# Kernel optimization log

Measured on AMD Instinct MI355X. Metric: run time of the kernel, lower is better.

Reference implementation:

```python
import jax, jax.numpy as jnp
import numpy as np

N_NODES = 50000
N_EDGES = 800000
F_IN = 64
F_HID = 64
K = 3


def _cheb_norm(edge_index, edge_weight, n):
    # PyG ChebConv sym normalization with lambda_max=2: Lhat = -D^{-1/2} A D^{-1/2}
    # (diagonal of Lhat is exactly 0, so self-loop terms vanish)
    row, col = edge_index[0], edge_index[1]
    deg = jax.ops.segment_sum(edge_weight, row, num_segments=n)
    dis = jnp.where(deg > 0, jax.lax.rsqrt(jnp.where(deg > 0, deg, 1.0)), 0.0)
    return -dis[row] * edge_weight * dis[col]


def _prop(x, row, col, norm, n):
    # out[i] = sum_{e: col[e]=i} norm[e] * x[row[e]]
    return jax.ops.segment_sum(x[row] * norm[:, None], col, num_segments=n)


def _cheb_conv(x, W, b, row, col, norm, n):
    # ChebConv K=3: Tx0=x, Tx1=Lhat x, Tx2=2 Lhat Tx1 - Tx0
    tx0 = x
    tx1 = _prop(x, row, col, norm, n)
    tx2 = 2.0 * _prop(tx1, row, col, norm, n) - tx0
    return tx0 @ W[0] + tx1 @ W[1] + tx2 @ W[2] + b


def setup_inputs() -> dict:
    key = jax.random.key(0)
    ks = jax.random.split(key, 20)
    inp = {
        "x": jax.random.normal(ks[0], (N_NODES, F_IN), dtype=jnp.float32),
        "edge_index": jax.random.randint(ks[1], (2, N_EDGES), 0, N_NODES, dtype=jnp.int32),
        "edge_weight": jax.random.uniform(ks[2], (N_EDGES,), dtype=jnp.float32),
    }
    # 6 ChebConvs: x->gate (F_IN->F_HID) and h->gate (F_HID->F_HID) for z, r, h
    names_in = [("Wxz", "bxz", F_IN), ("Whz", "bhz", F_HID), ("Wxr", "bxr", F_IN),
                ("Whr", "bhr", F_HID), ("Wxh", "bxh", F_IN), ("Whh", "bhh", F_HID)]
    for i, (wn, bn, fin) in enumerate(names_in):
        scale = 1.0 / np.sqrt(fin)
        inp[wn] = jax.random.normal(ks[3 + i], (K, fin, F_HID), dtype=jnp.float32) * scale
        inp[bn] = jnp.zeros((F_HID,), dtype=jnp.float32)
    inp["Wlin"] = jax.random.normal(ks[12], (F_HID, 2), dtype=jnp.float32) * (1.0 / np.sqrt(F_HID))
    inp["blin"] = jnp.zeros((2,), dtype=jnp.float32)
    return inp


def reference(x, edge_index, edge_weight, Wxz, bxz, Whz, bhz, Wxr, bxr, Whr, bhr,
              Wxh, bxh, Whh, bhh, Wlin, blin):
    n = x.shape[0]
    row, col = edge_index[0], edge_index[1]
    norm = _cheb_norm(edge_index, edge_weight, n)
    h0 = jnp.zeros((n, F_HID), dtype=x.dtype)
    # GConvGRU single step (initial hidden state = 0)
    z = jax.nn.sigmoid(_cheb_conv(x, Wxz, bxz, row, col, norm, n)
                       + _cheb_conv(h0, Whz, bhz, row, col, norm, n))
    r = jax.nn.sigmoid(_cheb_conv(x, Wxr, bxr, row, col, norm, n)
                       + _cheb_conv(h0, Whr, bhr, row, col, norm, n))
    h_tilde = jnp.tanh(_cheb_conv(x, Wxh, bxh, row, col, norm, n)
                       + _cheb_conv(h0 * r, Whh, bhh, row, col, norm, n))
    h = z * h0 + (1.0 - z) * h_tilde
    # head: dropout in eval mode (identity) -> tanh -> linear -> sigmoid
    return jax.nn.sigmoid(jnp.tanh(h) @ Wlin + blin)
```

## Files before the change

kernel.cpp:

```cpp
#include <hip/hip_runtime.h>
#include <hip/hip_bf16.h>

#define N_NODES 50000
#define N_EDGES 800000
#define NB1 400
#define CH  2000
#define NBKT 196
#define CAP 8192
#define SORT_MAX 6144

typedef unsigned short ushort_t;
typedef unsigned long long u64;
typedef __attribute__((ext_vector_type(8))) short bf16x8;
typedef __attribute__((ext_vector_type(4))) float f32x4;

constexpr int GCUR_O  = 0;
constexpr int DIS_O   = 512;
constexpr int OFF_O   = 50512;
constexpr int CSLOT_O = 100544;
constexpr int RSLOT_O = 3311808;
constexpr int RW_O    = 4917440;
constexpr int ABUF_O  = 6517440;
constexpr int PBUF_O  = 11317440;
constexpr int XS_O    = CSLOT_O;
constexpr int T1S_O   = RSLOT_O;

__device__ __forceinline__ ushort_t f32_to_bf16(float f) {
    unsigned u = __float_as_uint(f);
    u += 0x7fffu + ((u >> 16) & 1u);
    return (ushort_t)(u >> 16);
}
__device__ __forceinline__ float bflo(unsigned u) { return __uint_as_float(u << 16); }
__device__ __forceinline__ float bfhi(unsigned u) { return __uint_as_float(u & 0xffff0000u); }
__device__ __forceinline__ unsigned packbf2(float a, float b) {
    return (unsigned)f32_to_bf16(a) | ((unsigned)f32_to_bf16(b) << 16);
}
__device__ __forceinline__ float fsigmoid(float x) { return 1.f / (1.f + __expf(-x)); }
__device__ __forceinline__ float ftanh(float x) {
    x = fminf(15.f, fmaxf(-15.f, x));
    float e = __expf(2.f * x);
    return (e - 1.f) / (e + 1.f);
}

__global__ __launch_bounds__(512) void k1(
    const int* __restrict__ ei, const float* __restrict__ ew,
    const float* __restrict__ x, const float* __restrict__ Wxz,
    const float* __restrict__ Wxh, unsigned* __restrict__ gcur,
    u64* __restrict__ cslot, unsigned* __restrict__ rslot,
    unsigned* __restrict__ abuf, ushort_t* __restrict__ pbuf) {
    int bid = blockIdx.x, t = threadIdx.x;
    if (bid < NB1) {
        __shared__ unsigned colbuf[CH], rowbuf[CH];
        __shared__ unsigned hc[256], hr[256], bc[256], br[256];
        if (t < 256) { hc[t] = 0; hr[t] = 0; }
        __syncthreads();
        int e0 = bid * CH;
        for (int i = t; i < CH; i += 512) {
            unsigned r = (unsigned)ei[e0 + i];
            unsigned c = (unsigned)ei[N_EDGES + e0 + i];
            rowbuf[i] = r;
            colbuf[i] = c;
            atomicAdd(&hc[c >> 8], 1u);
            atomicAdd(&hr[r >> 8], 1u);
        }
        __syncthreads();
        if (t < NBKT) {
            bc[t] = atomicAdd(&gcur[t], hc[t]);
            br[t] = atomicAdd(&gcur[256 + t], hr[t]);
        }
        __syncthreads();
        if (t < 256) { hc[t] = 0; hr[t] = 0; }
        __syncthreads();
        for (int i = t; i < CH; i += 512) {
            unsigned c = colbuf[i];
            unsigned r = rowbuf[i];
            unsigned w = __float_as_uint(ew[e0 + i]);
            unsigned dc = c >> 8;
            unsigned pc = bc[dc] + atomicAdd(&hc[dc], 1u);
            if (pc < CAP)
                cslot[dc * CAP + pc] = ((u64)w << 32) | ((c & 255u) << 16) | (r & 0xFFFFu);
            unsigned dr = r >> 8;
            unsigned pr = br[dr] + atomicAdd(&hr[dr], 1u);
            if (pr < CAP) rslot[dr * CAP + pr] = (w & 0xFFFFFF00u) | (r & 255u);
        }
    } else if (bid < NB1 + 98) {
        int n0 = (bid - NB1) * 512;
        for (int idx = t; idx < 512 * 32; idx += 512) {
            int n = n0 + (idx >> 5);
            if (n < N_NODES) {
                int q = idx & 31;
                float2 xv = ((const float2*)x)[n * 32 + q];
                abuf[n * 96 + q] = packbf2(xv.x, xv.y);
            }
        }
    } else {
        for (int idx = t; idx < 24576; idx += 512) {
            int k = idx >> 7, n = idx & 127;
            float v = (n < 64) ? Wxz[k * 64 + n] : Wxh[k * 64 + (n - 64)];
            int c = n >> 4, s = k >> 5, l = (((k >> 3) & 3) << 4) | (n & 15), j = k & 7;
            pbuf[((c * 6 + s) * 64 + l) * 8 + j] = f32_to_bf16(v);
        }
    }
}

__global__ __launch_bounds__(512) void k2(
    const float* __restrict__ x, const unsigned* __restrict__ gcur,
    const u64* __restrict__ cslot, const unsigned* __restrict__ rslot,
    float* __restrict__ dis, int* __restrict__ off,
    u64* __restrict__ rw, unsigned* __restrict__ xs) {
    int bid = blockIdx.x, t = threadIdx.x;
    __shared__ unsigned rawA[SORT_MAX], rawB[SORT_MAX];
    __shared__ unsigned hist[256], hsc[256], cur[256], gs[256];
    __shared__ float facc[256];

    if (t < 256) {
        gs[t] = (t < NBKT) ? gcur[t] : 0u;
        hist[t] = 0;
    }
    __syncthreads();
    for (int o = 1; o < 256; o <<= 1) {
        unsigned v = (t < 256 && t >= o) ? gs[t - o] : 0u;
        __syncthreads();
        if (t < 256) gs[t] += v;
        __syncthreads();
    }
    unsigned szb = gcur[bid];
    unsigned sz = min(szb, (unsigned)SORT_MAX);
    unsigned base = gs[bid] - szb;
    for (unsigned i = t; i < sz; i += 512) {
        u64 v = cslot[bid * CAP + i];
        unsigned lo = (unsigned)v;
        rawA[i] = lo;
        rawB[i] = (unsigned)(v >> 32);
        atomicAdd(&hist[(lo >> 16) & 255u], 1u);
    }
    __syncthreads();
    unsigned h0 = (t < 256) ? hist[t] : 0u;
    if (t < 256) hsc[t] = h0;
    __syncthreads();
    for (int o = 1; o < 256; o <<= 1) {
        unsigned v = (t < 256 && t >= o) ? hsc[t - o] : 0u;
        __syncthreads();
        if (t < 256) hsc[t] += v;
        __syncthreads();
    }
    if (t < 256) {
        hsc[t] -= h0;
        cur[t] = 0u;
        int c = bid * 256 + t;
        if (c <= N_NODES) off[c] = (int)(base + hsc[t]);
    }
    __syncthreads();
    for (unsigned i = t; i < sz; i += 512) {
        unsigned lo = rawA[i];
        unsigned d = (lo >> 16) & 255u;
        unsigned p = hsc[d] + atomicAdd(&cur[d], 1u);
        rw[base + p] = ((u64)rawB[i] << 32) | (lo & 0xFFFFu);
    }
    __syncthreads();

    if (t < 256) facc[t] = 0.f;
    __syncthreads();
    unsigned szr = min(gcur[256 + bid], (unsigned)CAP);
    for (unsigned i = t; i < szr; i += 512) {
        unsigned v = rslot[bid * CAP + i];
        atomicAdd(&facc[v & 255u], __uint_as_float(v & 0xFFFFFF00u));
    }
    __syncthreads();
    if (t < 256) {
        float d = facc[t];
        float r = d > 0.f ? rsqrtf(d) : 0.f;
        facc[t] = r;
        int n = bid * 256 + t;
        if (n < N_NODES) dis[n] = r;
    }
    __syncthreads();
    for (int idx = t; idx < 8192; idx += 512) {
        int nl = idx >> 5, q = idx & 31;
        int n = bid * 256 + nl;
        if (n < N_NODES) {
            float2 xv = ((const float2*)x)[n * 32 + q];
            float r = facc[nl];
            xs[n * 32 + q] = packbf2(r * xv.x, r * xv.y);
        }
    }
}

__global__ __launch_bounds__(256) void k_prop(
    const int* __restrict__ off, const u64* __restrict__ rw,
    const unsigned* __restrict__ xsrc, const float* __restrict__ dis,
    const float* __restrict__ xf, unsigned* __restrict__ abuf,
    unsigned* __restrict__ t1s, int mode) {
    int node = (blockIdx.x * 256 + threadIdx.x) >> 6;
    if (node >= N_NODES) return;
    int lane = threadIdx.x & 63, h = lane >> 5, q = lane & 31;
    int b = off[node], end = off[node + 1];
    float acc0 = 0.f, acc1 = 0.f;
    for (; b + 7 < end; b += 8) {
        u64 v0 = rw[b + h], v1 = rw[b + h + 2], v2 = rw[b + h + 4], v3 = rw[b + h + 6];
        unsigned r0 = (unsigned)v0 & 0xFFFFu, r1 = (unsigned)v1 & 0xFFFFu;
        unsigned r2 = (unsigned)v2 & 0xFFFFu, r3 = (unsigned)v3 & 0xFFFFu;
        float a0 = __uint_as_float((unsigned)(v0 >> 32));
        float a1 = __uint_as_float((unsigned)(v1 >> 32));
        float a2 = __uint_as_float((unsigned)(v2 >> 32));
        float a3 = __uint_as_float((unsigned)(v3 >> 32));
        unsigned u0 = xsrc[r0 * 32 + q], u1 = xsrc[r1 * 32 + q];
        unsigned u2 = xsrc[r2 * 32 + q], u3 = xsrc[r3 * 32 + q];
        acc0 += a0 * bflo(u0) + a1 * bflo(u1) + a2 * bflo(u2) + a3 * bflo(u3);
        acc1 += a0 * bfhi(u0) + a1 * bfhi(u1) + a2 * bfhi(u2) + a3 * bfhi(u3);
    }
    for (; b + 1 < end; b += 2) {
        u64 v = rw[b + h];
        unsigned r = (unsigned)v & 0xFFFFu;
        float a = __uint_as_float((unsigned)(v >> 32));
        unsigned u = xsrc[r * 32 + q];
        acc0 += a * bflo(u); acc1 += a * bfhi(u);
    }
    if (b < end && h == 0) {
        u64 v = rw[b];
        unsigned r = (unsigned)v & 0xFFFFu;
        float a = __uint_as_float((unsigned)(v >> 32));
        unsigned u = xsrc[r * 32 + q];
        acc0 += a * bflo(u); acc1 += a * bfhi(u);
    }
    acc0 += __shfl_xor(acc0, 32, 64);
    acc1 += __shfl_xor(acc1, 32, 64);
    if (h == 0) {
        float di = dis[node];
        float t0 = -di * acc0, t1v = -di * acc1;
        if (mode == 0) {
            abuf[node * 96 + 32 + q] = packbf2(t0, t1v);
            t1s[node * 32 + q] = packbf2(di * t0, di * t1v);
        } else {
            float2 xv = ((const float2*)xf)[node * 32 + q];
            abuf[node * 96 + 64 + q] = packbf2(2.f * t0 - xv.x, 2.f * t1v - xv.y);
        }
    }
}

__global__ __launch_bounds__(256) void k_gemm(
    const ushort_t* __restrict__ ab, const ushort_t* __restrict__ pbuf,
    const float* __restrict__ bxz, const float* __restrict__ bhz,
    const float* __restrict__ bxh, const float* __restrict__ bhh,
    const float* __restrict__ Wlin, const float* __restrict__ blin,
    float2* __restrict__ out) {
    __shared__ ushort_t bsh[24576];
    int tid = threadIdx.x;
    {
        uint4* s4 = (uint4*)bsh;
        const uint4* g4 = (const uint4*)pbuf;
        for (int i = tid; i < 3072; i += 256) s4[i] = g4[i];
    }
    __syncthreads();

    int wave = tid >> 6, lane = tid & 63;
    int quad = lane >> 4, m = lane & 15;
    int arow = blockIdx.x * 64 + wave * 16 + m;
    const ushort_t* ap = ab + (size_t)arow * 192 + quad * 8;

    f32x4 acc[8];
#pragma unroll
    for (int c = 0; c < 8; ++c) acc[c] = (f32x4){0.f, 0.f, 0.f, 0.f};
#pragma unroll
    for (int s = 0; s < 6; ++s) {
        bf16x8 af = *(const bf16x8*)(ap + s * 32);
#pragma unroll
        for (int c = 0; c < 8; ++c) {
            bf16x8 bfr = *(const bf16x8*)(bsh + ((c * 6 + s) * 64 + lane) * 8);
            acc[c] = __builtin_amdgcn_mfma_f32_16x16x32_bf16(af, bfr, acc[c], 0, 0, 0);
        }
    }
    float bzv[4], bhv[4], wl0[4], wl1[4];
#pragma unroll
    for (int c = 0; c < 4; ++c) {
        int col = c * 16 + m;
        bzv[c] = bxz[col] + bhz[col];
        bhv[c] = bxh[col] + bhh[col];
        wl0[c] = Wlin[2 * col];
        wl1[c] = Wlin[2 * col + 1];
    }
    float bl0 = blin[0], bl1 = blin[1];
#pragma unroll
    for (int i = 0; i < 4; ++i) {
        float p0 = 0.f, p1 = 0.f;
#pragma unroll
        for (int c = 0; c < 4; ++c) {
            float z  = fsigmoid(acc[c][i] + bzv[c]);
            float ht = ftanh(acc[c + 4][i] + bhv[c]);
            float t  = ftanh((1.f - z) * ht);
            p0 += t * wl0[c];
            p1 += t * wl1[c];
        }
        for (int o = 1; o <= 8; o <<= 1) {
            p0 += __shfl_xor(p0, o, 64);
            p1 += __shfl_xor(p1, o, 64);
        }
        int g = blockIdx.x * 64 + wave * 16 + quad * 4 + i;
        if (m == 0 && g < N_NODES)
            out[g] = make_float2(fsigmoid(p0 + bl0), fsigmoid(p1 + bl1));
    }
}

extern "C" void kernel_launch(void* const* d_in, const int* in_sizes, int n_in,
                              void* d_out, int out_size, void* d_ws, size_t ws_size,
                              hipStream_t stream) {
    const float* x    = (const float*)d_in[0];
    const int*   ei   = (const int*)d_in[1];
    const float* ew   = (const float*)d_in[2];
    const float* Wxz  = (const float*)d_in[3];
    const float* bxz  = (const float*)d_in[4];
    const float* bhz  = (const float*)d_in[6];
    const float* Wxh  = (const float*)d_in[11];
    const float* bxh  = (const float*)d_in[12];
    const float* bhh  = (const float*)d_in[14];
    const float* Wlin = (const float*)d_in[15];
    const float* blin = (const float*)d_in[16];

    float*    ws    = (float*)d_ws;
    unsigned* gcur  = (unsigned*)(ws + GCUR_O);
    float*    dis   = ws + DIS_O;
    int*      off   = (int*)(ws + OFF_O);
    u64*      cslot = (u64*)(ws + CSLOT_O);
    unsigned* rslot = (unsigned*)(ws + RSLOT_O);
    u64*      rw    = (u64*)(ws + RW_O);
    unsigned* abuf  = (unsigned*)(ws + ABUF_O);
    ushort_t* pbuf  = (ushort_t*)(ws + PBUF_O);
    unsigned* xs    = (unsigned*)(ws + XS_O);
    unsigned* t1s   = (unsigned*)(ws + T1S_O);

    hipMemsetAsync(d_ws, 0, 512 * 4, stream);

    k1<<<NB1 + 98 + 1, 512, 0, stream>>>(ei, ew, x, Wxz, Wxh, gcur, cslot, rslot, abuf, pbuf);
    k2<<<NBKT, 512, 0, stream>>>(x, gcur, cslot, rslot, dis, off, rw, xs);
    k_prop<<<12500, 256, 0, stream>>>(off, rw, xs, dis, x, abuf, t1s, 0);
    k_prop<<<12500, 256, 0, stream>>>(off, rw, t1s, dis, x, abuf, abuf, 1);
    k_gemm<<<782, 256, 0, stream>>>((const ushort_t*)abuf, pbuf, bxz, bhz, bxh, bhh,
                                    Wlin, blin, (float2*)d_out);
}
```

Measured before the change: 219.2 us.

## Replace CSR sort with bucketed shared-memory atomic scatter propagation

Measured after the change: 851.2 us. 288% more time.

```diff
diff --git a/kernel.cpp b/kernel.cpp
--- a/kernel.cpp
+++ b/kernel.cpp
@@ -5,9 +5,8 @@
 #define N_EDGES 800000
 #define NB1 400
 #define CH  2000
-#define NBKT 196
-#define CAP 8192
-#define SORT_MAX 6144
+#define NBKT 391
+#define CAP 4096
 
 typedef unsigned short ushort_t;
 typedef unsigned long long u64;
@@ -15,15 +14,13 @@
 typedef __attribute__((ext_vector_type(4))) float f32x4;
 
 constexpr int GCUR_O  = 0;
-constexpr int DIS_O   = 512;
-constexpr int OFF_O   = 50512;
-constexpr int CSLOT_O = 100544;
-constexpr int RSLOT_O = 3311808;
-constexpr int RW_O    = 4917440;
-constexpr int ABUF_O  = 6517440;
-constexpr int PBUF_O  = 11317440;
-constexpr int XS_O    = CSLOT_O;
-constexpr int T1S_O   = RSLOT_O;
+constexpr int DIS_O   = 12544;
+constexpr size_t CSLOT_O = 62592;
+constexpr size_t RSLOT_O = 3265664;
+constexpr size_t XS_O    = 4867200;
+constexpr size_t T1S_O   = 6467200;
+constexpr size_t ABUF_O  = 8067200;
+constexpr size_t PBUF_O  = 12871808;
 
 __device__ __forceinline__ ushort_t f32_to_bf16(float f) {
     unsigned u = __float_as_uint(f);
@@ -44,15 +41,14 @@
 
 __global__ __launch_bounds__(512) void k1(
     const int* __restrict__ ei, const float* __restrict__ ew,
-    const float* __restrict__ x, const float* __restrict__ Wxz,
-    const float* __restrict__ Wxh, unsigned* __restrict__ gcur,
-    u64* __restrict__ cslot, unsigned* __restrict__ rslot,
-    unsigned* __restrict__ abuf, ushort_t* __restrict__ pbuf) {
+    const float* __restrict__ Wxz, const float* __restrict__ Wxh,
+    unsigned* __restrict__ gcur, u64* __restrict__ cslot,
+    unsigned* __restrict__ rslot, ushort_t* __restrict__ pbuf) {
     int bid = blockIdx.x, t = threadIdx.x;
     if (bid < NB1) {
         __shared__ unsigned colbuf[CH], rowbuf[CH];
-        __shared__ unsigned hc[256], hr[256], bc[256], br[256];
-        if (t < 256) { hc[t] = 0; hr[t] = 0; }
+        __shared__ unsigned hc[NBKT], hr[NBKT], bc[NBKT], br[NBKT];
+        if (t < NBKT) { hc[t] = 0; hr[t] = 0; }
         __syncthreads();
         int e0 = bid * CH;
         for (int i = t; i < CH; i += 512) {
@@ -60,38 +56,29 @@
             unsigned c = (unsigned)ei[N_EDGES + e0 + i];
             rowbuf[i] = r;
             colbuf[i] = c;
-            atomicAdd(&hc[c >> 8], 1u);
-            atomicAdd(&hr[r >> 8], 1u);
+            atomicAdd(&hc[c >> 7], 1u);
+            atomicAdd(&hr[r >> 7], 1u);
         }
         __syncthreads();
         if (t < NBKT) {
-            bc[t] = atomicAdd(&gcur[t], hc[t]);
-            br[t] = atomicAdd(&gcur[256 + t], hr[t]);
-        }
-        __syncthreads();
-        if (t < 256) { hc[t] = 0; hr[t] = 0; }
+            bc[t] = atomicAdd(&gcur[t * 16], hc[t]);
+            br[t] = atomicAdd(&gcur[(NBKT + t) * 16], hr[t]);
+        }
+        __syncthreads();
+        if (t < NBKT) { hc[t] = 0; hr[t] = 0; }
         __syncthreads();
         for (int i = t; i < CH; i += 512) {
             unsigned c = colbuf[i];
             unsigned r = rowbuf[i];
             unsigned w = __float_as_uint(ew[e0 + i]);
-            unsigned dc = c >> 8;
+            unsigned dc = c >> 7;
             unsigned pc = bc[dc] + atomicAdd(&hc[dc], 1u);
             if (pc < CAP)
-                cslot[dc * CAP + pc] = ((u64)w << 32) | ((c & 255u) << 16) | (r & 0xFFFFu);
-            unsigned dr = r >> 8;
+                cslot[(size_t)dc * CAP + pc] = ((u64)w << 32) | ((c & 127u) << 16) | (r & 0xFFFFu);
+            unsigned dr = r >> 7;
             unsigned pr = br[dr] + atomicAdd(&hr[dr], 1u);
-            if (pr < CAP) rslot[dr * CAP + pr] = (w & 0xFFFFFF00u) | (r & 255u);
-        }
-    } else if (bid < NB1 + 98) {
-        int n0 = (bid - NB1) * 512;
-        for (int idx = t; idx < 512 * 32; idx += 512) {
-            int n = n0 + (idx >> 5);
-            if (n < N_NODES) {
-                int q = idx & 31;
-                float2 xv = ((const float2*)x)[n * 32 + q];
-                abuf[n * 96 + q] = packbf2(xv.x, xv.y);
-            }
+            if (pr < CAP)
+                rslot[(size_t)dr * CAP + pr] = (w & 0xFFFFFF80u) | (r & 127u);
         }
     } else {
         for (int idx = t; idx < 24576; idx += 512) {
@@ -105,135 +92,95 @@
 
 __global__ __launch_bounds__(512) void k2(
     const float* __restrict__ x, const unsigned* __restrict__ gcur,
-    const u64* __restrict__ cslot, const unsigned* __restrict__ rslot,
-    float* __restrict__ dis, int* __restrict__ off,
-    u64* __restrict__ rw, unsigned* __restrict__ xs) {
+    const unsigned* __restrict__ rslot, float* __restrict__ dis,
+    unsigned* __restrict__ abuf, unsigned* __restrict__ xs) {
     int bid = blockIdx.x, t = threadIdx.x;
-    __shared__ unsigned rawA[SORT_MAX], rawB[SORT_MAX];
-    __shared__ unsigned hist[256], hsc[256], cur[256], gs[256];
-    __shared__ float facc[256];
-
-    if (t < 256) {
-        gs[t] = (t < NBKT) ? gcur[t] : 0u;
-        hist[t] = 0;
-    }
-    __syncthreads();
-    for (int o = 1; o < 256; o <<= 1) {
-        unsigned v = (t < 256 && t >= o) ? gs[t - o] : 0u;
-        __syncthreads();
-        if (t < 256) gs[t] += v;
-        __syncthreads();
-    }
-    unsigned szb = gcur[bid];
-    unsigned sz = min(szb, (unsigned)SORT_MAX);
-    unsigned base = gs[bid] - szb;
-    for (unsigned i = t; i < sz; i += 512) {
-        u64 v = cslot[bid * CAP + i];
-        unsigned lo = (unsigned)v;
-        rawA[i] = lo;
-        rawB[i] = (unsigned)(v >> 32);
-        atomicAdd(&hist[(lo >> 16) & 255u], 1u);
-    }
-    __syncthreads();
-    unsigned h0 = (t < 256) ? hist[t] : 0u;
-    if (t < 256) hsc[t] = h0;
-    __syncthreads();
-    for (int o = 1; o < 256; o <<= 1) {
-        unsigned v = (t < 256 && t >= o) ? hsc[t - o] : 0u;
-        __syncthreads();
-        if (t < 256) hsc[t] += v;
-        __syncthreads();
-    }
-    if (t < 256) {
-        hsc[t] -= h0;
-        cur[t] = 0u;
-        int c = bid * 256 + t;
-        if (c <= N_NODES) off[c] = (int)(base + hsc[t]);
-    }
-    __syncthreads();
-    for (unsigned i = t; i < sz; i += 512) {
-        unsigned lo = rawA[i];
-        unsigned d = (lo >> 16) & 255u;
-        unsigned p = hsc[d] + atomicAdd(&cur[d], 1u);
-        rw[base + p] = ((u64)rawB[i] << 32) | (lo & 0xFFFFu);
-    }
-    __syncthreads();
-
-    if (t < 256) facc[t] = 0.f;
-    __syncthreads();
-    unsigned szr = min(gcur[256 + bid], (unsigned)CAP);
-    for (unsigned i = t; i < szr; i += 512) {
-        unsigned v = rslot[bid * CAP + i];
-        atomicAdd(&facc[v & 255u], __uint_as_float(v & 0xFFFFFF00u));
-    }
-    __syncthreads();
-    if (t < 256) {
+    __shared__ float facc[128];
+    if (t < 128) facc[t] = 0.f;
+    __syncthreads();
+    unsigned szr = min(gcur[(NBKT + bid) * 16], (unsigned)CAP);
+    const unsigned* rs = rslot + (size_t)bid * CAP;
+    for (unsigned i = t; i < szr; i += 512)
+        atomicAdd(&facc[rs[i] & 127u], __uint_as_float(rs[i] & 0xFFFFFF80u));
+    __syncthreads();
+    if (t < 128) {
         float d = facc[t];
         float r = d > 0.f ? rsqrtf(d) : 0.f;
         facc[t] = r;
-        int n = bid * 256 + t;
+        int n = bid * 128 + t;
         if (n < N_NODES) dis[n] = r;
     }
     __syncthreads();
-    for (int idx = t; idx < 8192; idx += 512) {
+    for (int idx = t; idx < 128 * 32; idx += 512) {
         int nl = idx >> 5, q = idx & 31;
-        int n = bid * 256 + nl;
+        int n = bid * 128 + nl;
         if (n < N_NODES) {
-            float2 xv = ((const float2*)x)[n * 32 + q];
             float r = facc[nl];
-            xs[n * 32 + q] = packbf2(r * xv.x, r * xv.y);
-        }
-    }
-}
-
-__global__ __launch_bounds__(256) void k_prop(
-    const int* __restrict__ off, const u64* __restrict__ rw,
-    const unsigned* __restrict__ xsrc, const float* __restrict__ dis,
-    const float* __restrict__ xf, unsigned* __restrict__ abuf,
+            float2 xp = ((const float2*)x)[n * 32 + q];
+            abuf[n * 96 + q] = packbf2(xp.x, xp.y);
+            float xa = x[n * 64 + q], xb = x[n * 64 + q + 32];
+            xs[n * 32 + q] = packbf2(r * xa, r * xb);
+        }
+    }
+}
+
+__global__ __launch_bounds__(512) void k_prop(
+    const unsigned* __restrict__ gcur, const u64* __restrict__ cslot,
+    const unsigned* __restrict__ src, const float* __restrict__ dis,
+    const float* __restrict__ x, unsigned* __restrict__ abuf,
     unsigned* __restrict__ t1s, int mode) {
-    int node = (blockIdx.x * 256 + threadIdx.x) >> 6;
-    if (node >= N_NODES) return;
-    int lane = threadIdx.x & 63, h = lane >> 5, q = lane & 31;
-    int b = off[node], end = off[node + 1];
-    float acc0 = 0.f, acc1 = 0.f;
-    for (; b + 7 < end; b += 8) {
-        u64 v0 = rw[b + h], v1 = rw[b + h + 2], v2 = rw[b + h + 4], v3 = rw[b + h + 6];
-        unsigned r0 = (unsigned)v0 & 0xFFFFu, r1 = (unsigned)v1 & 0xFFFFu;
-        unsigned r2 = (unsigned)v2 & 0xFFFFu, r3 = (unsigned)v3 & 0xFFFFu;
-        float a0 = __uint_as_float((unsigned)(v0 >> 32));
-        float a1 = __uint_as_float((unsigned)(v1 >> 32));
-        float a2 = __uint_as_float((unsigned)(v2 >> 32));
-        float a3 = __uint_as_float((unsigned)(v3 >> 32));
-        unsigned u0 = xsrc[r0 * 32 + q], u1 = xsrc[r1 * 32 + q];
-        unsigned u2 = xsrc[r2 * 32 + q], u3 = xsrc[r3 * 32 + q];
-        acc0 += a0 * bflo(u0) + a1 * bflo(u1) + a2 * bflo(u2) + a3 * bflo(u3);
-        acc1 += a0 * bfhi(u0) + a1 * bfhi(u1) + a2 * bfhi(u2) + a3 * bfhi(u3);
-    }
-    for (; b + 1 < end; b += 2) {
-        u64 v = rw[b + h];
-        unsigned r = (unsigned)v & 0xFFFFu;
-        float a = __uint_as_float((unsigned)(v >> 32));
-        unsigned u = xsrc[r * 32 + q];
-        acc0 += a * bflo(u); acc1 += a * bfhi(u);
-    }
-    if (b < end && h == 0) {
-        u64 v = rw[b];
-        unsigned r = (unsigned)v & 0xFFFFu;
-        float a = __uint_as_float((unsigned)(v >> 32));
-        unsigned u = xsrc[r * 32 + q];
-        acc0 += a * bflo(u); acc1 += a * bfhi(u);
-    }
-    acc0 += __shfl_xor(acc0, 32, 64);
-    acc1 += __shfl_xor(acc1, 32, 64);
-    if (h == 0) {
-        float di = dis[node];
-        float t0 = -di * acc0, t1v = -di * acc1;
-        if (mode == 0) {
-            abuf[node * 96 + 32 + q] = packbf2(t0, t1v);
-            t1s[node * 32 + q] = packbf2(di * t0, di * t1v);
-        } else {
-            float2 xv = ((const float2*)xf)[node * 32 + q];
-            abuf[node * 96 + 64 + q] = packbf2(2.f * t0 - xv.x, 2.f * t1v - xv.y);
+    __shared__ float tile[128 * 64];
+    int bid = blockIdx.x, t = threadIdx.x;
+    for (int i = t; i < 8192; i += 512) tile[i] = 0.f;
+    __syncthreads();
+    unsigned sz = min(gcur[bid * 16], (unsigned)CAP);
+    const u64* cs = cslot + (size_t)bid * CAP;
+    int lane = t & 63, wv = t >> 6;
+    int h = lane >> 5, q = lane & 31;
+    unsigned i0 = wv * 8 + h * 4;
+    unsigned szf = sz & ~63u;
+    for (unsigned i = i0; i < szf; i += 64) {
+        ulonglong2 pA = *(const ulonglong2*)(cs + i);
+        ulonglong2 pB = *(const ulonglong2*)(cs + i + 2);
+#pragma unroll
+        for (int j = 0; j < 4; ++j) {
+            u64 p = (j == 0) ? pA.x : (j == 1) ? pA.y : (j == 2) ? pB.x : pB.y;
+            unsigned lo = (unsigned)p;
+            float w = __uint_as_float((unsigned)(p >> 32));
+            unsigned c = (lo >> 16) & 127u;
+            unsigned r = lo & 0xFFFFu;
+            unsigned u = src[r * 32 + q];
+            atomicAdd(&tile[c * 64 + q], w * bflo(u));
+            atomicAdd(&tile[c * 64 + q + 32], w * bfhi(u));
+        }
+    }
+    for (unsigned e = szf + (unsigned)(wv * 2 + h); e < sz; e += 16) {
+        u64 p = cs[e];
+        unsigned lo = (unsigned)p;
+        float w = __uint_as_float((unsigned)(p >> 32));
+        unsigned c = (lo >> 16) & 127u;
+        unsigned r = lo & 0xFFFFu;
+        unsigned u = src[r * 32 + q];
+        atomicAdd(&tile[c * 64 + q], w * bflo(u));
+        atomicAdd(&tile[c * 64 + q + 32], w * bfhi(u));
+    }
+    __syncthreads();
+    for (int idx = t; idx < 128 * 32; idx += 512) {
+        int nl = idx >> 5, q2 = idx & 31;
+        int n = bid * 128 + nl;
+        if (n < N_NODES) {
+            float di = dis[n];
+            float s0 = tile[nl * 64 + 2 * q2], s1 = tile[nl * 64 + 2 * q2 + 1];
+            if (mode == 0) {
+                abuf[n * 96 + 32 + q2] = packbf2(-di * s0, -di * s1);
+                float u0 = tile[nl * 64 + q2], u1 = tile[nl * 64 + q2 + 32];
+                float d2 = -di * di;
+                t1s[n * 32 + q2] = packbf2(d2 * u0, d2 * u1);
+            } else {
+                float2 xp = ((const float2*)x)[n * 32 + q2];
+                abuf[n * 96 + 64 + q2] = packbf2(-2.f * di * s0 - xp.x,
+                                                 -2.f * di * s1 - xp.y);
+            }
         }
     }
 }
@@ -319,21 +266,19 @@
     float*    ws    = (float*)d_ws;
     unsigned* gcur  = (unsigned*)(ws + GCUR_O);
     float*    dis   = ws + DIS_O;
-    int*      off   = (int*)(ws + OFF_O);
     u64*      cslot = (u64*)(ws + CSLOT_O);
     unsigned* rslot = (unsigned*)(ws + RSLOT_O);
-    u64*      rw    = (u64*)(ws + RW_O);
+    unsigned* xs    = (unsigned*)(ws + XS_O);
+    unsigned* t1s   = (unsigned*)(ws + T1S_O);
     unsigned* abuf  = (unsigned*)(ws + ABUF_O);
     ushort_t* pbuf  = (ushort_t*)(ws + PBUF_O);
-    unsigned* xs    = (unsigned*)(ws + XS_O);
-    unsigned* t1s   = (unsigned*)(ws + T1S_O);
-
-    hipMemsetAsync(d_ws, 0, 512 * 4, stream);
-
-    k1<<<NB1 + 98 + 1, 512, 0, stream>>>(ei, ew, x, Wxz, Wxh, gcur, cslot, rslot, abuf, pbuf);
-    k2<<<NBKT, 512, 0, stream>>>(x, gcur, cslot, rslot, dis, off, rw, xs);
-    k_prop<<<12500, 256, 0, stream>>>(off, rw, xs, dis, x, abuf, t1s, 0);
-    k_prop<<<12500, 256, 0, stream>>>(off, rw, t1s, dis, x, abuf, abuf, 1);
+
+    hipMemsetAsync(d_ws, 0, (size_t)(782 * 16) * 4, stream);
+
+    k1<<<NB1 + 1, 512, 0, stream>>>(ei, ew, Wxz, Wxh, gcur, cslot, rslot, pbuf);
+    k2<<<NBKT, 512, 0, stream>>>(x, gcur, rslot, dis, abuf, xs);
+    k_prop<<<NBKT, 512, 0, stream>>>(gcur, cslot, xs, dis, x, abuf, t1s, 0);
+    k_prop<<<NBKT, 512, 0, stream>>>(gcur, cslot, t1s, dis, x, abuf, t1s, 1);
     k_gemm<<<782, 256, 0, stream>>>((const ushort_t*)abuf, pbuf, bxz, bhz, bxh, bhh,
                                     Wlin, blin, (float2*)d_out);
 }
```
